# Kernel tuning notes

Hardware: AMD Instinct MI355X
Metric: run time of the kernel (lower is better)

The kernel has to match this reference:

```python
import jax, jax.numpy as jnp
import numpy as np

N = 50000      # batch_node_num (unique nodes)
E = 800000     # number of edges (avg degree 16)
IN = 128       # in_dim
OUT = 128      # out_dim
B = 10000      # query nodes


def setup_inputs() -> dict:
    key = jax.random.key(0)
    k = jax.random.split(key, 8)
    edges = jax.random.randint(k[0], (E, 2), 0, N, dtype=jnp.int64)
    node_idx = jax.random.randint(k[1], (B,), 0, N, dtype=jnp.int64)
    local_features = jax.random.normal(k[2], (N, IN), dtype=jnp.float32)
    W1 = jax.random.normal(k[3], (IN, OUT), dtype=jnp.float32) * (1.0 / np.sqrt(IN))
    b1 = jnp.zeros((OUT,), dtype=jnp.float32)
    W2 = jax.random.normal(k[4], (OUT, OUT), dtype=jnp.float32) * (1.0 / np.sqrt(OUT))
    b2 = jnp.zeros((OUT,), dtype=jnp.float32)
    return {"edges": edges, "node_idx": node_idx, "local_features": local_features,
            "W1": W1, "b1": b1, "W2": W2, "b2": b2, "ind": 2}


def reference(edges, node_idx, local_features, W1, b1, W2, b2, ind):
    mask = jnp.array([1.0, 1.0, 0.0, 0.0], dtype=jnp.float32)
    # Linear -> Tanh -> Linear (the out_linear_layer MLP)
    h = jnp.tanh(local_features @ W1 + b1) @ W2 + b2          # [N, OUT]
    src, dst = edges[:, 0], edges[:, 1]
    # self-loop edges get weight mask[ind], others weight 1
    values = jnp.where(src == dst, mask[ind], jnp.float32(1.0))  # [E]
    # spmm(matrix, ones) == per-row degree (weighted)
    row_sum = jax.ops.segment_sum(values, src, num_segments=N)   # [N]
    row_sum = jnp.where(row_sum == 0, jnp.float32(1.0), row_sum)
    # spmm(matrix, new_embeddings): gather dst embeddings, scatter-add to src
    results = jax.ops.segment_sum(values[:, None] * h[dst], src, num_segments=N)  # [N, OUT]
    output_emb = results / row_sum[:, None]
    return output_emb[node_idx]
```

## Files before the change

### kernel.cpp

```cpp
#include <hip/hip_runtime.h>

#define IN_DIM 128
#define CAP 128
#define LDT 136
#define SCAT_BLOCKS 384

typedef short v8s __attribute__((ext_vector_type(8)));
typedef float v4f __attribute__((ext_vector_type(4)));

__device__ inline unsigned short f2bf(float f) {
    unsigned int u = __float_as_uint(f);
    u += 0x7FFFu + ((u >> 16) & 1u);
    return (unsigned short)(u >> 16);
}
__device__ inline float bf2f(unsigned short h) {
    return __uint_as_float((unsigned int)h << 16);
}

__global__ __launch_bounds__(256) void prep(
    const float* __restrict__ W1, const float* __restrict__ W2,
    unsigned short* __restrict__ Wt1, unsigned short* __restrict__ Wt2,
    const int* __restrict__ node_idx, int* __restrict__ flag, int B,
    int* __restrict__ cursor, int N, int nbF)
{
    int bid = blockIdx.x;
    if (bid < 128) {
        int i = bid * 256 + threadIdx.x;
        int m = i >> 14, rem = i & 16383;
        int n = rem >> 7, k = rem & 127;
        float wv = (m ? W2 : W1)[k * 128 + n];
        int idx = n * 128 + (((k >> 3) ^ (n & 15)) << 3) + (k & 7);
        (m ? Wt2 : Wt1)[idx] = f2bf(wv);
    } else if (bid < 128 + nbF) {
        int i = (bid - 128) * 256 + threadIdx.x;
        if (i < B) flag[node_idx[i]] = 1;
    } else {
        int i = (bid - 128 - nbF) * 256 + threadIdx.x;
        if (i < N) cursor[i] = 0;
    }
}

__global__ __launch_bounds__(256, 2) void mlp_fill(
    const float* __restrict__ X,
    const unsigned short* __restrict__ Wt1, const unsigned short* __restrict__ Wt2,
    const float* __restrict__ b1, const float* __restrict__ b2,
    unsigned short* __restrict__ Hb, int nrows,
    const int* __restrict__ edges, const int* __restrict__ flag,
    const int* __restrict__ indp, int* __restrict__ cursor,
    unsigned short* __restrict__ col, int E, int mlpBlocks)
{
    const int bid = blockIdx.x;

    if (bid >= mlpBlocks) {
        const int keepSelf = (*indp < 2) ? 1 : 0;
        const int stride = SCAT_BLOCKS * 256;
        for (int e = (bid - mlpBlocks) * 256 + threadIdx.x; e < E; e += stride) {
            int2 ed = ((const int2*)edges)[e];
            if ((ed.x != ed.y || keepSelf) && flag[ed.x] == 1) {
                int p = atomicAdd(&cursor[ed.x], 1);
                if (p < CAP)
                    col[(size_t)ed.x * CAP + p] = (unsigned short)ed.y;
            }
        }
        return;
    }

    __shared__ uint4 Wl4[2048];
    __shared__ unsigned short Ts[4 * 32 * LDT];
    const unsigned short* Wls = (const unsigned short*)Wl4;
    const int t    = threadIdx.x;
    const int w    = t >> 6;
    const int lane = t & 63;
    const int l15  = lane & 15;
    const int quad = lane >> 4;
    const int R0   = bid * 128;
    const int wrow = w * 32;
    unsigned short* Tw = &Ts[w * 32 * LDT];

    int gr0 = R0 + wrow + l15;        gr0 = gr0 < nrows ? gr0 : nrows - 1;
    int gr1 = R0 + wrow + 16 + l15;   gr1 = gr1 < nrows ? gr1 : nrows - 1;
    const float* xrow[2] = { &X[(size_t)gr0 * 128 + quad * 8],
                             &X[(size_t)gr1 * 128 + quad * 8] };

#pragma unroll
    for (int j = 0; j < 8; ++j)
        Wl4[j * 256 + t] = ((const uint4*)Wt1)[j * 256 + t];

    v4f acc[2][8];
#pragma unroll
    for (int rt = 0; rt < 2; ++rt)
#pragma unroll
        for (int ct = 0; ct < 8; ++ct)
            acc[rt][ct] = (v4f){0.f, 0.f, 0.f, 0.f};

    __syncthreads();

#pragma unroll
    for (int kk = 0; kk < 4; ++kk) {
        v8s Bf[8];
#pragma unroll
        for (int ct = 0; ct < 8; ++ct)
            Bf[ct] = *(const v8s*)
                &Wls[(ct * 16 + l15) * 128 + (((kk * 4 + quad) ^ l15) * 8)];
        v8s Ar[2];
#pragma unroll
        for (int rt = 0; rt < 2; ++rt) {
            const float* xp = xrow[rt] + kk * 32;
            float4 x0 = *(const float4*)xp;
            float4 x1 = *(const float4*)(xp + 4);
            v8s av;
            av[0] = (short)f2bf(x0.x); av[1] = (short)f2bf(x0.y);
            av[2] = (short)f2bf(x0.z); av[3] = (short)f2bf(x0.w);
            av[4] = (short)f2bf(x1.x); av[5] = (short)f2bf(x1.y);
            av[6] = (short)f2bf(x1.z); av[7] = (short)f2bf(x1.w);
            Ar[rt] = av;
        }
#pragma unroll
        for (int ct = 0; ct < 8; ++ct)
#pragma unroll
            for (int rt = 0; rt < 2; ++rt)
                acc[rt][ct] = __builtin_amdgcn_mfma_f32_16x16x32_bf16(
                    Ar[rt], Bf[ct], acc[rt][ct], 0, 0, 0);
    }
#pragma unroll
    for (int ct = 0; ct < 8; ++ct) {
        float bias = b1[ct * 16 + l15];
#pragma unroll
        for (int rt = 0; rt < 2; ++rt) {
#pragma unroll
            for (int r = 0; r < 4; ++r)
                Tw[(rt * 16 + quad * 4 + r) * LDT + ct * 16 + l15] =
                    f2bf(tanhf(acc[rt][ct][r] + bias));
            acc[rt][ct] = (v4f){0.f, 0.f, 0.f, 0.f};
        }
    }

    __syncthreads();
#pragma unroll
    for (int j = 0; j < 8; ++j)
        Wl4[j * 256 + t] = ((const uint4*)Wt2)[j * 256 + t];
    __syncthreads();

#pragma unroll
    for (int kk = 0; kk < 4; ++kk) {
        v8s Bf[8];
#pragma unroll
        for (int ct = 0; ct < 8; ++ct)
            Bf[ct] = *(const v8s*)
                &Wls[(ct * 16 + l15) * 128 + (((kk * 4 + quad) ^ l15) * 8)];
        v8s Ar[2];
#pragma unroll
        for (int rt = 0; rt < 2; ++rt)
            Ar[rt] = *(const v8s*)
                &Tw[(rt * 16 + l15) * LDT + kk * 32 + quad * 8];
#pragma unroll
        for (int ct = 0; ct < 8; ++ct)
#pragma unroll
            for (int rt = 0; rt < 2; ++rt)
                acc[rt][ct] = __builtin_amdgcn_mfma_f32_16x16x32_bf16(
                    Ar[rt], Bf[ct], acc[rt][ct], 0, 0, 0);
    }
    asm volatile("s_waitcnt lgkmcnt(0)" ::: "memory");
#pragma unroll
    for (int ct = 0; ct < 8; ++ct) {
        float bias = b2[ct * 16 + l15];
#pragma unroll
        for (int rt = 0; rt < 2; ++rt)
#pragma unroll
            for (int r = 0; r < 4; ++r)
                Tw[(rt * 16 + quad * 4 + r) * LDT + ct * 16 + l15] =
                    f2bf(acc[rt][ct][r] + bias);
    }
    asm volatile("s_waitcnt lgkmcnt(0)" ::: "memory");
#pragma unroll
    for (int i = 0; i < 8; ++i) {
        int lr = i * 4 + quad;
        int c  = l15;
        uint4 v = *(const uint4*)&Tw[lr * LDT + c * 8];
        int grow = R0 + wrow + lr;
        if (grow < nrows)
            *(uint4*)&Hb[(size_t)grow * 128 + c * 8] = v;
    }
}

__global__ __launch_bounds__(256) void aggregate_out(
    const int* __restrict__ node_idx, const int* __restrict__ cursor,
    const unsigned short* __restrict__ col, const unsigned short* __restrict__ Hb,
    float* __restrict__ out, int B)
{
    int b = (int)((blockIdx.x * blockDim.x + threadIdx.x) >> 6);
    if (b >= B) return;
    int lane = threadIdx.x & 63;
    int v = node_idx[b];
    int deg = cursor[v];
    deg = deg < CAP ? deg : CAP;
    const unsigned short* cp = &col[(size_t)v * CAP];
    int myc = (lane < deg) ? (int)cp[lane] : 0;
    int dmax = deg < 64 ? deg : 64;
    float ax = 0.f, ay = 0.f, bx = 0.f, by = 0.f;
    int i = 0;
    for (; i + 1 < dmax; i += 2) {
        int d0 = __shfl(myc, i, 64);
        int d1 = __shfl(myc, i + 1, 64);
        unsigned int u0 = *(const unsigned int*)&Hb[(size_t)d0 * 128 + lane * 2];
        unsigned int u1 = *(const unsigned int*)&Hb[(size_t)d1 * 128 + lane * 2];
        ax += bf2f((unsigned short)(u0 & 0xFFFFu));
        ay += bf2f((unsigned short)(u0 >> 16));
        bx += bf2f((unsigned short)(u1 & 0xFFFFu));
        by += bf2f((unsigned short)(u1 >> 16));
    }
    if (i < dmax) {
        int d0 = __shfl(myc, i, 64);
        unsigned int u0 = *(const unsigned int*)&Hb[(size_t)d0 * 128 + lane * 2];
        ax += bf2f((unsigned short)(u0 & 0xFFFFu));
        ay += bf2f((unsigned short)(u0 >> 16));
    }
    for (int j = 64; j < deg; ++j) {
        int d0 = cp[j];
        unsigned int u0 = *(const unsigned int*)&Hb[(size_t)d0 * 128 + lane * 2];
        ax += bf2f((unsigned short)(u0 & 0xFFFFu));
        ay += bf2f((unsigned short)(u0 >> 16));
    }
    float den = (deg > 0) ? (float)deg : 1.0f;
    *(float2*)&out[(size_t)b * 128 + lane * 2] =
        make_float2((ax + bx) / den, (ay + by) / den);
}

extern "C" void kernel_launch(void* const* d_in, const int* in_sizes, int n_in,
                              void* d_out, int out_size, void* d_ws, size_t ws_size,
                              hipStream_t stream)
{
    const int*   edges    = (const int*)d_in[0];
    const int*   node_idx = (const int*)d_in[1];
    const float* X        = (const float*)d_in[2];
    const float* W1       = (const float*)d_in[3];
    const float* b1       = (const float*)d_in[4];
    const float* W2       = (const float*)d_in[5];
    const float* b2       = (const float*)d_in[6];
    const int*   indp     = (const int*)d_in[7];

    const int E = in_sizes[0] / 2;
    const int B = in_sizes[1];
    const int N = in_sizes[2] / IN_DIM;
    const int mlpBlocks = (N + 127) / 128;
    const int nbF = (B + 255) / 256;
    const int nbC = (N + 255) / 256;

    char* ws = (char*)d_ws;
    size_t off = 0;
    int* cursor = (int*)(ws + off); off += (size_t)N * 4;
    int* flag   = (int*)(ws + off); off += (size_t)N * 4;
    off = (off + 15) & ~(size_t)15;
    unsigned short* Hb  = (unsigned short*)(ws + off); off += (size_t)N * IN_DIM * 2;
    unsigned short* col = (unsigned short*)(ws + off); off += (size_t)N * CAP * 2;
    unsigned short* Wt1 = (unsigned short*)(ws + off); off += 16384 * 2;
    unsigned short* Wt2 = (unsigned short*)(ws + off); off += 16384 * 2;

    hipLaunchKernelGGL(prep, dim3(128 + nbF + nbC), dim3(256), 0, stream,
                       W1, W2, Wt1, Wt2, node_idx, flag, B, cursor, N, nbF);
    hipLaunchKernelGGL(mlp_fill, dim3(mlpBlocks + SCAT_BLOCKS), dim3(256),
                       0, stream, X, Wt1, Wt2, b1, b2, Hb, N,
                       edges, flag, indp, cursor, col, E, mlpBlocks);
    hipLaunchKernelGGL(aggregate_out, dim3((B * 64 + 255) / 256), dim3(256), 0,
                       stream, node_idx, cursor, col, Hb, (float*)d_out, B);
}
```

Baseline: 121.9 us.

## Prepack weights in MFMA fragment order and read them directly from global memory

The prep kernel now writes W1/W2 as bf16 in the exact per-lane MFMA B-fragment order, so each wave loads its B operands straight from global or L2 memory with coalesced 16-byte reads. This removes the shared-memory weight staging and its block barriers, and shrinks LDS use so launch bounds can rise to 3 blocks per SIMD. tanhf is also replaced by an exp2/rcp approximation. In exchange, every wave re-reads the 64KB of weights from cache, and the tanh loses some precision.

Result: faster. 116.5 us (-4.5%).

```diff
diff --git a/kernel.cpp b/kernel.cpp
--- a/kernel.cpp
+++ b/kernel.cpp
@@ -16,21 +16,30 @@
 __device__ inline float bf2f(unsigned short h) {
     return __uint_as_float((unsigned int)h << 16);
 }
+__device__ inline float fast_tanh(float x) {
+    float e = __builtin_amdgcn_exp2f(x * 2.885390081777927f);
+    return 1.0f - 2.0f * __builtin_amdgcn_rcpf(e + 1.0f);
+}
 
 __global__ __launch_bounds__(256) void prep(
     const float* __restrict__ W1, const float* __restrict__ W2,
-    unsigned short* __restrict__ Wt1, unsigned short* __restrict__ Wt2,
+    unsigned short* __restrict__ Wf1, unsigned short* __restrict__ Wf2,
     const int* __restrict__ node_idx, int* __restrict__ flag, int B,
     int* __restrict__ cursor, int N, int nbF)
 {
     int bid = blockIdx.x;
     if (bid < 128) {
         int i = bid * 256 + threadIdx.x;
-        int m = i >> 14, rem = i & 16383;
-        int n = rem >> 7, k = rem & 127;
+        int m = i >> 14, o = i & 16383;
+        int j   = o & 7;
+        int l15 = (o >> 3) & 15;
+        int quad = (o >> 7) & 3;
+        int ct  = (o >> 9) & 7;
+        int kk  = (o >> 12) & 3;
+        int k = kk * 32 + quad * 8 + j;
+        int n = ct * 16 + l15;
         float wv = (m ? W2 : W1)[k * 128 + n];
-        int idx = n * 128 + (((k >> 3) ^ (n & 15)) << 3) + (k & 7);
-        (m ? Wt2 : Wt1)[idx] = f2bf(wv);
+        (m ? Wf2 : Wf1)[o] = f2bf(wv);
     } else if (bid < 128 + nbF) {
         int i = (bid - 128) * 256 + threadIdx.x;
         if (i < B) flag[node_idx[i]] = 1;
@@ -40,9 +49,9 @@
     }
 }
 
-__global__ __launch_bounds__(256, 2) void mlp_fill(
+__global__ __launch_bounds__(256, 3) void mlp_fill(
     const float* __restrict__ X,
-    const unsigned short* __restrict__ Wt1, const unsigned short* __restrict__ Wt2,
+    const unsigned short* __restrict__ Wf1, const unsigned short* __restrict__ Wf2,
     const float* __restrict__ b1, const float* __restrict__ b2,
     unsigned short* __restrict__ Hb, int nrows,
     const int* __restrict__ edges, const int* __restrict__ flag,
@@ -65,9 +74,7 @@
         return;
     }
 
-    __shared__ uint4 Wl4[2048];
     __shared__ unsigned short Ts[4 * 32 * LDT];
-    const unsigned short* Wls = (const unsigned short*)Wl4;
     const int t    = threadIdx.x;
     const int w    = t >> 6;
     const int lane = t & 63;
@@ -82,9 +89,8 @@
     const float* xrow[2] = { &X[(size_t)gr0 * 128 + quad * 8],
                              &X[(size_t)gr1 * 128 + quad * 8] };
 
-#pragma unroll
-    for (int j = 0; j < 8; ++j)
-        Wl4[j * 256 + t] = ((const uint4*)Wt1)[j * 256 + t];
+    const v8s* Wp1 = (const v8s*)Wf1 + lane;
+    const v8s* Wp2 = (const v8s*)Wf2 + lane;
 
     v4f acc[2][8];
 #pragma unroll
@@ -93,15 +99,8 @@
         for (int ct = 0; ct < 8; ++ct)
             acc[rt][ct] = (v4f){0.f, 0.f, 0.f, 0.f};
 
-    __syncthreads();
-
 #pragma unroll
     for (int kk = 0; kk < 4; ++kk) {
-        v8s Bf[8];
-#pragma unroll
-        for (int ct = 0; ct < 8; ++ct)
-            Bf[ct] = *(const v8s*)
-                &Wls[(ct * 16 + l15) * 128 + (((kk * 4 + quad) ^ l15) * 8)];
         v8s Ar[2];
 #pragma unroll
         for (int rt = 0; rt < 2; ++rt) {
@@ -116,11 +115,13 @@
             Ar[rt] = av;
         }
 #pragma unroll
-        for (int ct = 0; ct < 8; ++ct)
-#pragma unroll
-            for (int rt = 0; rt < 2; ++rt)
-                acc[rt][ct] = __builtin_amdgcn_mfma_f32_16x16x32_bf16(
-                    Ar[rt], Bf[ct], acc[rt][ct], 0, 0, 0);
+        for (int ct = 0; ct < 8; ++ct) {
+            v8s Bfc = Wp1[(kk * 8 + ct) * 64];
+            acc[0][ct] = __builtin_amdgcn_mfma_f32_16x16x32_bf16(
+                Ar[0], Bfc, acc[0][ct], 0, 0, 0);
+            acc[1][ct] = __builtin_amdgcn_mfma_f32_16x16x32_bf16(
+                Ar[1], Bfc, acc[1][ct], 0, 0, 0);
+        }
     }
 #pragma unroll
     for (int ct = 0; ct < 8; ++ct) {
@@ -130,35 +131,27 @@
 #pragma unroll
             for (int r = 0; r < 4; ++r)
                 Tw[(rt * 16 + quad * 4 + r) * LDT + ct * 16 + l15] =
-                    f2bf(tanhf(acc[rt][ct][r] + bias));
+                    f2bf(fast_tanh(acc[rt][ct][r] + bias));
             acc[rt][ct] = (v4f){0.f, 0.f, 0.f, 0.f};
         }
     }
 
-    __syncthreads();
-#pragma unroll
-    for (int j = 0; j < 8; ++j)
-        Wl4[j * 256 + t] = ((const uint4*)Wt2)[j * 256 + t];
-    __syncthreads();
 
 #pragma unroll
     for (int kk = 0; kk < 4; ++kk) {
-        v8s Bf[8];
-#pragma unroll
-        for (int ct = 0; ct < 8; ++ct)
-            Bf[ct] = *(const v8s*)
-                &Wls[(ct * 16 + l15) * 128 + (((kk * 4 + quad) ^ l15) * 8)];
         v8s Ar[2];
 #pragma unroll
         for (int rt = 0; rt < 2; ++rt)
             Ar[rt] = *(const v8s*)
                 &Tw[(rt * 16 + l15) * LDT + kk * 32 + quad * 8];
 #pragma unroll
-        for (int ct = 0; ct < 8; ++ct)
-#pragma unroll
-            for (int rt = 0; rt < 2; ++rt)
-                acc[rt][ct] = __builtin_amdgcn_mfma_f32_16x16x32_bf16(
-                    Ar[rt], Bf[ct], acc[rt][ct], 0, 0, 0);
+        for (int ct = 0; ct < 8; ++ct) {
+            v8s Bfc = Wp2[(kk * 8 + ct) * 64];
+            acc[0][ct] = __builtin_amdgcn_mfma_f32_16x16x32_bf16(
+                Ar[0], Bfc, acc[0][ct], 0, 0, 0);
+            acc[1][ct] = __builtin_amdgcn_mfma_f32_16x16x32_bf16(
+                Ar[1], Bfc, acc[1][ct], 0, 0, 0);
+        }
     }
     asm volatile("s_waitcnt lgkmcnt(0)" ::: "memory");
 #pragma unroll
@@ -253,13 +246,13 @@
     off = (off + 15) & ~(size_t)15;
     unsigned short* Hb  = (unsigned short*)(ws + off); off += (size_t)N * IN_DIM * 2;
     unsigned short* col = (unsigned short*)(ws + off); off += (size_t)N * CAP * 2;
-    unsigned short* Wt1 = (unsigned short*)(ws + off); off += 16384 * 2;
-    unsigned short* Wt2 = (unsigned short*)(ws + off); off += 16384 * 2;
+    unsigned short* Wf1 = (unsigned short*)(ws + off); off += 16384 * 2;
+    unsigned short* Wf2 = (unsigned short*)(ws + off); off += 16384 * 2;
 
     hipLaunchKernelGGL(prep, dim3(128 + nbF + nbC), dim3(256), 0, stream,
-                       W1, W2, Wt1, Wt2, node_idx, flag, B, cursor, N, nbF);
+                       W1, W2, Wf1, Wf2, node_idx, flag, B, cursor, N, nbF);
     hipLaunchKernelGGL(mlp_fill, dim3(mlpBlocks + SCAT_BLOCKS), dim3(256),
-                       0, stream, X, Wt1, Wt2, b1, b2, Hb, N,
+                       0, stream, X, Wf1, Wf2, b1, b2, Hb, N,
                        edges, flag, indp, cursor, col, E, mlpBlocks);
     hipLaunchKernelGGL(aggregate_out, dim3((B * 64 + 255) / 256), dim3(256), 0,
                        stream, node_idx, cursor, col, Hb, (float*)d_out, B);
```
